# Kernel optimization log

Measured on AMD Instinct MI355X. Metric: run time of the kernel, lower is better.

The kernel has to match this reference:

```python
import jax, jax.numpy as jnp
import numpy as np

P = 32            # patch_num_row
KS = 5            # kernel_size
DIM = 1024
HEADS = 16
DIM_HEAD = 64
INNER = HEADS * DIM_HEAD
SCALE = DIM_HEAD ** -0.5


def _nearby_mask(p=P, ks=KS):
    # True = masked out (matches torch masked_fill semantics)
    pad = ks // 2
    m = np.ones((p * p, p + 2 * pad, p + 2 * pad), dtype=bool)
    for i in range(p):
        for j in range(p):
            m[i * p + j, i:i + ks, j:j + ks] = False
    m = m[:, pad:-pad, pad:-pad].reshape(p * p, p * p)
    # F.pad(mask, (1,0,1,0), value=False): unmasked first row/col (BOS token)
    m = np.pad(m, ((1, 0), (1, 0)), constant_values=False)
    return jnp.asarray(m)  # [n, n], n = p*p + 1

NB_MASK = _nearby_mask()


def setup_inputs() -> dict:
    key = jax.random.key(0)
    ks = jax.random.split(key, 8)
    b, n = 16, P * P + 1
    s = DIM ** -0.5
    return {
        "q": jax.random.normal(ks[0], (b, n, DIM), jnp.float32),
        "k": jax.random.normal(ks[1], (b, n, DIM), jnp.float32),
        "v": jax.random.normal(ks[2], (b, n, DIM), jnp.float32),
        "Wq": jax.random.normal(ks[3], (DIM, INNER), jnp.float32) * s,
        "Wk": jax.random.normal(ks[4], (DIM, INNER), jnp.float32) * s,
        "Wv": jax.random.normal(ks[5], (DIM, INNER), jnp.float32) * s,
        "Wo": jax.random.normal(ks[6], (INNER, DIM), jnp.float32) * (INNER ** -0.5),
        "bo": jnp.zeros((DIM,), jnp.float32),
    }


def reference(q, k, v, Wq, Wk, Wv, Wo, bo):
    b, n, _ = q.shape
    h, d = HEADS, DIM_HEAD
    # projections, split heads: b n (h d) -> b h n d
    qh = (q @ Wq).reshape(b, n, h, d).transpose(0, 2, 1, 3)
    kh = (k @ Wk).reshape(b, n, h, d).transpose(0, 2, 1, 3)
    vh = (v @ Wv).reshape(b, n, h, d).transpose(0, 2, 1, 3)
    dots = jnp.einsum('bhid,bhjd->bhij', qh, kh) * SCALE
    mask_value = -jnp.finfo(dots.dtype).max
    dots = jnp.where(NB_MASK[None, None], mask_value, dots)
    attn = jax.nn.softmax(dots, axis=-1)
    out = jnp.einsum('bhij,bhjd->bhid', attn, vh)
    out = out.transpose(0, 2, 1, 3).reshape(b, n, h * d)
    return out @ Wo + bo
```

## Files before the change

### kernel.cpp

```cpp
#include <hip/hip_runtime.h>

typedef unsigned short u16;
typedef unsigned int   u32;
typedef __attribute__((ext_vector_type(8))) __bf16 bf16x8;
typedef __attribute__((ext_vector_type(4))) float   f32x4;

#define MROWS 16400
#define NPADROWS 16512
#define KD 1024
#define MATEL ((size_t)NPADROWS * KD)
#define NT 16
#define BUFSZ 16384

__device__ __forceinline__ u16 f2b(float f) {
  union { float f; u32 u; } x; x.f = f;
  return (u16)((x.u + 0x7FFFu + ((x.u >> 16) & 1u)) >> 16);
}
__device__ __forceinline__ float b2f(u16 h) {
  union { u32 u; float f; } x; x.u = ((u32)h) << 16;
  return x.f;
}

__device__ __forceinline__ void gll16(const u16* g, u16* l) {
  __builtin_amdgcn_global_load_lds(
      (const __attribute__((address_space(1))) void*)g,
      (__attribute__((address_space(3))) void*)l, 16, 0, 0);
}

__global__ __launch_bounds__(256) void k_wtrans(
    const float* __restrict__ W0, const float* __restrict__ W1,
    const float* __restrict__ W2, const float* __restrict__ W3,
    u16* __restrict__ T)
{
  __shared__ float tile[32][33];
  int z = blockIdx.z;
  const float* W = (z == 0) ? W0 : (z == 1) ? W1 : (z == 2) ? W2 : W3;
  u16* Tz = T + (size_t)z * KD * KD;
  int tx = threadIdx.x, ty = threadIdx.y;
  int k0 = blockIdx.x * 32, n0 = blockIdx.y * 32;
#pragma unroll
  for (int r = ty; r < 32; r += 8)
    tile[r][tx] = W[(size_t)(k0 + r) * KD + n0 + tx];
  __syncthreads();
#pragma unroll
  for (int r = ty; r < 32; r += 8)
    Tz[(size_t)(n0 + r) * KD + k0 + tx] = f2b(tile[tx][r]);
}

__global__ __launch_bounds__(256) void k_convert(
    const float* __restrict__ q, const float* __restrict__ k,
    const float* __restrict__ v, u16* __restrict__ dst)
{
  const size_t CH_PER_MAT = MATEL / 8;
  const size_t total = 3 * CH_PER_MAT;
  for (size_t c = (size_t)blockIdx.x * 256 + threadIdx.x; c < total;
       c += (size_t)gridDim.x * 256) {
    size_t z = c / CH_PER_MAT;
    size_t r = c - z * CH_PER_MAT;
    size_t row = r >> 7;
    int col8 = (int)(r & 127) * 8;
    u16* o = dst + z * MATEL + row * KD + col8;
    if (row < MROWS) {
      const float* s = ((z == 0) ? q : (z == 1) ? k : v) + row * KD + col8;
      float4 f0 = *(const float4*)s;
      float4 f1 = *(const float4*)(s + 4);
      ushort4 o0; o0.x = f2b(f0.x); o0.y = f2b(f0.y); o0.z = f2b(f0.z); o0.w = f2b(f0.w);
      ushort4 o1; o1.x = f2b(f1.x); o1.y = f2b(f1.y); o1.z = f2b(f1.z); o1.w = f2b(f1.w);
      *(ushort4*)o = o0; *(ushort4*)(o + 4) = o1;
    } else {
      ushort4 zz; zz.x = zz.y = zz.z = zz.w = 0;
      *(ushort4*)o = zz; *(ushort4*)(o + 4) = zz;
    }
  }
}

template<bool OUT_FP32>
__global__ __launch_bounds__(256) void k_gemm(
    const u16* __restrict__ Ab, const u16* __restrict__ Bt,
    u16* __restrict__ Cb, float* __restrict__ Cf,
    const float* __restrict__ bias, int nwg)
{
  __shared__ u16 lds[2 * BUFSZ];

  int lin = blockIdx.x;
  int cpx = nwg >> 3;
  int swz = (lin & 7) * cpx + (lin >> 3);
  int bn = swz & 7;
  int rest = swz >> 3;
  int bm = rest % 129;
  int z  = rest / 129;

  int t = threadIdx.x;
  int w = t >> 6, l = t & 63;
  int lrow = l & 15, kgrp = l >> 4;
  int wm = (w >> 1) * 64, wn = (w & 1) * 64;

  int ccl = ((t & 7) ^ ((t >> 3) & 7)) * 8;
  const u16* gA[4]; const u16* gB[4];
#pragma unroll
  for (int i = 0; i < 4; ++i) {
    int prow = i * 32 + (t >> 3);
    gA[i] = Ab + (size_t)z * MATEL + (size_t)(bm * 128 + prow) * KD + ccl;
    gB[i] = Bt + (size_t)z * (1024 * 1024) + (size_t)(bn * 128 + prow) * KD + ccl;
  }

  int aoff[4], boff[4];
#pragma unroll
  for (int fm = 0; fm < 4; ++fm)
    aoff[fm] = (wm + fm * 16 + lrow) * 64 + ((kgrp ^ (l & 7)) * 8);
#pragma unroll
  for (int fn = 0; fn < 4; ++fn)
    boff[fn] = 8192 + (wn + fn * 16 + lrow) * 64 + ((kgrp ^ (l & 7)) * 8);

  f32x4 acc[4][4] = {};

#define STAGE(B) { u16* L = lds + (B) * BUFSZ;                          \
    _Pragma("unroll")                                                   \
    for (int i = 0; i < 4; ++i) { gll16(gA[i], L + i * 2048 + w * 512); gA[i] += 64; } \
    _Pragma("unroll")                                                   \
    for (int i = 0; i < 4; ++i) { gll16(gB[i], L + 8192 + i * 2048 + w * 512); gB[i] += 64; } }

  STAGE(0);
  __syncthreads();

  int buf = 0;
#pragma unroll 2
  for (int kt = 0; kt < NT; ++kt) {
    if (kt + 1 < NT) STAGE(buf ^ 1);

    const u16* Lb = lds + buf * BUFSZ;
#pragma unroll
    for (int ks = 0; ks < 2; ++ks) {
      bf16x8 af[4], bfr[4];
#pragma unroll
      for (int fm = 0; fm < 4; ++fm)
        af[fm] = *(const bf16x8*)(Lb + (aoff[fm] ^ (ks << 5)));
#pragma unroll
      for (int fn = 0; fn < 4; ++fn)
        bfr[fn] = *(const bf16x8*)(Lb + (boff[fn] ^ (ks << 5)));
#pragma unroll
      for (int fm = 0; fm < 4; ++fm)
#pragma unroll
        for (int fn = 0; fn < 4; ++fn)
          acc[fm][fn] = __builtin_amdgcn_mfma_f32_16x16x32_bf16(af[fm], bfr[fn], acc[fm][fn], 0, 0, 0);
    }

    __syncthreads();
    buf ^= 1;
  }
#undef STAGE

#pragma unroll
  for (int fm = 0; fm < 4; ++fm) {
#pragma unroll
    for (int fn = 0; fn < 4; ++fn) {
      int gcol = bn * 128 + wn + fn * 16 + lrow;
#pragma unroll
      for (int r = 0; r < 4; ++r) {
        int grow = bm * 128 + wm + fm * 16 + kgrp * 4 + r;
        if constexpr (OUT_FP32) {
          if (grow < MROWS)
            Cf[(size_t)grow * KD + gcol] = acc[fm][fn][r] + bias[gcol];
        } else {
          Cb[(size_t)z * MATEL + (size_t)grow * KD + gcol] = f2b(acc[fm][fn][r]);
        }
      }
    }
  }
}

__global__ __launch_bounds__(256) void k_attn_nb22(
    const u16* __restrict__ Qp, const u16* __restrict__ Kp,
    const u16* __restrict__ Vp, u16* __restrict__ AO)
{
  __shared__ float qrow[4][1024];
  __shared__ float dots[4][16][37];
  __shared__ float probs[4][16][37];
  __shared__ int   keys[37];
  __shared__ unsigned long long incm[4];

  int t = threadIdx.x;
  int b = blockIdx.x >> 8;
  int tile = blockIdx.x & 255;
  int pi0 = (tile >> 4) * 2, pj0 = (tile & 15) * 2;
  size_t rowbase = (size_t)b * 1025;

  int iq[4];
#pragma unroll
  for (int qi = 0; qi < 4; ++qi)
    iq[qi] = 1 + (pi0 + (qi >> 1)) * 32 + (pj0 + (qi & 1));

  {
    int qi = t >> 6, off = (t & 63) * 16;
    const u16* qp = Qp + (rowbase + iq[qi]) * 1024 + off;
    uint4 a0 = *(const uint4*)qp;
    uint4 a1 = *(const uint4*)(qp + 8);
    u32 uu[8] = {a0.x, a0.y, a0.z, a0.w, a1.x, a1.y, a1.z, a1.w};
#pragma unroll
    for (int u = 0; u < 8; ++u) {
      qrow[qi][off + u * 2]     = __uint_as_float(uu[u] << 16);
      qrow[qi][off + u * 2 + 1] = __uint_as_float(uu[u] & 0xffff0000u);
    }
  }
  if (t < 37) {
    if (t < 36) {
      int r = pi0 - 2 + t / 6, c = pj0 - 2 + t % 6;
      keys[t] = (r >= 0 && r < 32 && c >= 0 && c < 32) ? (1 + r * 32 + c) : -1;
    } else {
      keys[36] = 0;
    }
  }
  if (t < 4) {
    int di = t >> 1, dj = t & 1;
    unsigned long long m = 1ull << 36;
    for (int j = 0; j < 36; ++j) {
      int wr = j / 6, wc = j % 6;
      if (wr >= di && wr < di + 5 && wc >= dj && wc < dj + 5) m |= 1ull << j;
    }
    incm[t] = m;
  }
  __syncthreads();

  int e = t & 3;
  int hD = (t >> 2) & 15;
  float qreg[4][16];
#pragma unroll
  for (int qi = 0; qi < 4; ++qi)
#pragma unroll
    for (int u = 0; u < 16; ++u)
      qreg[qi][u] = qrow[qi][hD * 64 + e * 16 + u];

#pragma unroll
  for (int p = 0; p < 10; ++p) {
    int idx = p * 64 + (t >> 2);
    float s0 = 0.f, s1 = 0.f, s2 = 0.f, s3 = 0.f;
    int key = -1;
    if (idx < 592) {
      int j = idx >> 4;
      key = keys[j];
      if (key >= 0) {
        const u16* kp = Kp + (rowbase + key) * 1024 + hD * 64 + e * 16;
        uint4 kv0 = *(const uint4*)kp;
        uint4 kv1 = *(const uint4*)(kp + 8);
        u32 uu[8] = {kv0.x, kv0.y, kv0.z, kv0.w, kv1.x, kv1.y, kv1.z, kv1.w};
#pragma unroll
        for (int u = 0; u < 8; ++u) {
          float lo = __uint_as_float(uu[u] << 16);
          float hi = __uint_as_float(uu[u] & 0xffff0000u);
          s0 += qreg[0][u * 2] * lo + qreg[0][u * 2 + 1] * hi;
          s1 += qreg[1][u * 2] * lo + qreg[1][u * 2 + 1] * hi;
          s2 += qreg[2][u * 2] * lo + qreg[2][u * 2 + 1] * hi;
          s3 += qreg[3][u * 2] * lo + qreg[3][u * 2 + 1] * hi;
        }
      }
    }
    s0 += __shfl_xor(s0, 1); s0 += __shfl_xor(s0, 2);
    s1 += __shfl_xor(s1, 1); s1 += __shfl_xor(s1, 2);
    s2 += __shfl_xor(s2, 1); s2 += __shfl_xor(s2, 2);
    s3 += __shfl_xor(s3, 1); s3 += __shfl_xor(s3, 2);
    if (idx < 592) {
      int j = idx >> 4;
      float sv = (e == 0) ? s0 : (e == 1) ? s1 : (e == 2) ? s2 : s3;
      dots[e][hD][j] = (key >= 0) ? sv * 0.125f : -3.0e38f;
    }
  }
  __syncthreads();

  {
    int row = t >> 2;
    int qi = row >> 4, hh = row & 15;
    unsigned long long inc = incm[qi];
    float dv[10];
    float m = -3.0e38f;
#pragma unroll
    for (int s = 0; s < 10; ++s) {
      int j = e + s * 4;
      float d = -3.0e38f;
      if (j < 37) {
        d = dots[qi][hh][j];
        if (!((inc >> j) & 1)) d = -3.0e38f;
      }
      dv[s] = d;
      m = fmaxf(m, d);
    }
    m = fmaxf(m, __shfl_xor(m, 1));
    m = fmaxf(m, __shfl_xor(m, 2));
    float sum = 0.f;
    float pv[10];
#pragma unroll
    for (int s = 0; s < 10; ++s) {
      int j = e + s * 4;
      float p = (j < 37) ? __expf(dv[s] - m) : 0.f;
      pv[s] = p; sum += p;
    }
    sum += __shfl_xor(sum, 1);
    sum += __shfl_xor(sum, 2);
    float inv = 1.f / sum;
#pragma unroll
    for (int s = 0; s < 10; ++s) {
      int j = e + s * 4;
      if (j < 37) probs[qi][hh][j] = pv[s] * inv;
    }
  }
  __syncthreads();

  {
    int h = t >> 4;
    int c0 = t * 4;
    float a[4][4] = {};
    for (int j = 0; j < 37; ++j) {
      int key = keys[j];
      if (key < 0) continue;
      ushort4 vv = *(const ushort4*)(Vp + (rowbase + key) * 1024 + c0);
      float v0 = b2f(vv.x), v1 = b2f(vv.y), v2 = b2f(vv.z), v3 = b2f(vv.w);
#pragma unroll
      for (int qi = 0; qi < 4; ++qi) {
        float p = probs[qi][h][j];
        a[qi][0] += p * v0; a[qi][1] += p * v1;
        a[qi][2] += p * v2; a[qi][3] += p * v3;
      }
    }
#pragma unroll
    for (int qi = 0; qi < 4; ++qi) {
      ushort4 o;
      o.x = f2b(a[qi][0]); o.y = f2b(a[qi][1]);
      o.z = f2b(a[qi][2]); o.w = f2b(a[qi][3]);
      *(ushort4*)&AO[(rowbase + iq[qi]) * 1024 + c0] = o;
    }
  }
}

__global__ __launch_bounds__(256) void k_attn_row0(
    const u16* __restrict__ Qp, const u16* __restrict__ Kp,
    const u16* __restrict__ Vp, u16* __restrict__ AO)
{
  __shared__ float q0[64];
  __shared__ float pr[1025];
  __shared__ float red[256];
  int t = threadIdx.x;
  int b = blockIdx.x >> 4, h = blockIdx.x & 15;
  size_t rowbase = (size_t)b * 1025;

  if (t < 64) q0[t] = b2f(Qp[rowbase * 1024 + h * 64 + t]);
  __syncthreads();

  float lmax = -3.0e38f;
  for (int j = t; j < 1025; j += 256) {
    const u16* kp = Kp + (rowbase + j) * 1024 + h * 64;
    float s = 0.f;
#pragma unroll
    for (int e = 0; e < 64; e += 4) {
      ushort4 kv = *(const ushort4*)(kp + e);
      s += q0[e + 0] * b2f(kv.x) + q0[e + 1] * b2f(kv.y)
         + q0[e + 2] * b2f(kv.z) + q0[e + 3] * b2f(kv.w);
    }
    s *= 0.125f;
    pr[j] = s;
    lmax = fmaxf(lmax, s);
  }
  red[t] = lmax; __syncthreads();
  for (int s = 128; s > 0; s >>= 1) {
    if (t < s) red[t] = fmaxf(red[t], red[t + s]);
    __syncthreads();
  }
  float m = red[0]; __syncthreads();

  float lsum = 0.f;
  for (int j = t; j < 1025; j += 256) {
    float p = __expf(pr[j] - m);
    pr[j] = p; lsum += p;
  }
  red[t] = lsum; __syncthreads();
  for (int s = 128; s > 0; s >>= 1) {
    if (t < s) red[t] += red[t + s];
    __syncthreads();
  }
  float inv = 1.f / red[0]; __syncthreads();

  int d = t & 63, grp = t >> 6;
  float a = 0.f;
  for (int j = grp; j < 1025; j += 4)
    a += pr[j] * b2f(Vp[(rowbase + j) * 1024 + h * 64 + d]);
  red[t] = a; __syncthreads();
  if (t < 64) {
    float tot = (red[t] + red[t + 64]) + (red[t + 128] + red[t + 192]);
    AO[rowbase * 1024 + h * 64 + t] = f2b(tot * inv);
  }
}

extern "C" void kernel_launch(void* const* d_in, const int* in_sizes, int n_in,
                              void* d_out, int out_size, void* d_ws, size_t ws_size,
                              hipStream_t stream) {
  const float* q  = (const float*)d_in[0];
  const float* k  = (const float*)d_in[1];
  const float* v  = (const float*)d_in[2];
  const float* Wq = (const float*)d_in[3];
  const float* Wk = (const float*)d_in[4];
  const float* Wv = (const float*)d_in[5];
  const float* Wo = (const float*)d_in[6];
  const float* bo = (const float*)d_in[7];
  float* out = (float*)d_out;

  u16* wt = (u16*)d_ws;
  u16* qb = wt + (size_t)4 * 1024 * 1024;
  u16* Qp = qb + 3 * MATEL;
  u16* Kp = Qp + MATEL;
  u16* Vp = Kp + MATEL;
  u16* AO = qb;

  k_wtrans<<<dim3(32, 32, 4), dim3(32, 8), 0, stream>>>(Wq, Wk, Wv, Wo, wt);
  k_convert<<<2048, 256, 0, stream>>>(q, k, v, qb);

  k_gemm<false><<<3096, 256, 0, stream>>>(qb, wt, Qp, nullptr, nullptr, 3096);

  k_attn_nb22<<<4096, 256, 0, stream>>>(Qp, Kp, Vp, AO);
  k_attn_row0<<<256, 256, 0, stream>>>(Qp, Kp, Vp, AO);

  k_gemm<true><<<1032, 256, 0, stream>>>(AO, wt + (size_t)3 * 1024 * 1024,
                                         nullptr, out, bo, 1032);
}
```

Measured before the change: 433.2 us.

## Use 256x256 GEMM tiles with 512 threads and triple-buffered LDS pipeline

Replaces the 128x128 GEMM tile (256 threads, double buffer, K-step 64) with a 256x256 tile computed by 8 waves, K-step 32 and a three-stage LDS ring. Explicit vmcnt waits and raw barriers let two loads stay in flight, s_setprio raises MFMA priority, and an XCD-aware workgroup remap handles grid sizes not divisible by 8. The aim is more reuse of each loaded tile and better hiding of global-load latency. In exchange the block count drops to 780 and 260, which may underfill the GPU for the output projection, and register pressure rises with 32 accumulators per thread.

New measurement: 457.0 us. +5.5%, slower.

```diff
diff --git a/kernel.cpp b/kernel.cpp
--- a/kernel.cpp
+++ b/kernel.cpp
@@ -9,8 +9,6 @@
 #define NPADROWS 16512
 #define KD 1024
 #define MATEL ((size_t)NPADROWS * KD)
-#define NT 16
-#define BUFSZ 16384
 
 __device__ __forceinline__ u16 f2b(float f) {
   union { float f; u32 u; } x; x.f = f;
@@ -75,94 +73,115 @@
 }
 
 template<bool OUT_FP32>
-__global__ __launch_bounds__(256) void k_gemm(
+__global__ __launch_bounds__(512, 1) void k_gemm(
     const u16* __restrict__ Ab, const u16* __restrict__ Bt,
     u16* __restrict__ Cb, float* __restrict__ Cf,
     const float* __restrict__ bias, int nwg)
 {
-  __shared__ u16 lds[2 * BUFSZ];
+  __shared__ u16 lds[3 * 16384];
 
   int lin = blockIdx.x;
-  int cpx = nwg >> 3;
-  int swz = (lin & 7) * cpx + (lin >> 3);
-  int bn = swz & 7;
-  int rest = swz >> 3;
-  int bm = rest % 129;
-  int z  = rest / 129;
+  int qq = nwg >> 3, r8 = nwg & 7;
+  int xcd = lin & 7, pos = lin >> 3;
+  int wg = (xcd < r8 ? xcd * (qq + 1) : r8 * (qq + 1) + (xcd - r8) * qq) + pos;
+  int bn = wg & 3;
+  int rest = wg >> 2;
+  int bm = rest % 65;
+  int z  = rest / 65;
 
   int t = threadIdx.x;
   int w = t >> 6, l = t & 63;
   int lrow = l & 15, kgrp = l >> 4;
-  int wm = (w >> 1) * 64, wn = (w & 1) * 64;
-
-  int ccl = ((t & 7) ^ ((t >> 3) & 7)) * 8;
-  const u16* gA[4]; const u16* gB[4];
-#pragma unroll
-  for (int i = 0; i < 4; ++i) {
-    int prow = i * 32 + (t >> 3);
-    gA[i] = Ab + (size_t)z * MATEL + (size_t)(bm * 128 + prow) * KD + ccl;
-    gB[i] = Bt + (size_t)z * (1024 * 1024) + (size_t)(bn * 128 + prow) * KD + ccl;
-  }
-
-  int aoff[4], boff[4];
-#pragma unroll
-  for (int fm = 0; fm < 4; ++fm)
-    aoff[fm] = (wm + fm * 16 + lrow) * 64 + ((kgrp ^ (l & 7)) * 8);
-#pragma unroll
-  for (int fn = 0; fn < 4; ++fn)
-    boff[fn] = 8192 + (wn + fn * 16 + lrow) * 64 + ((kgrp ^ (l & 7)) * 8);
-
-  f32x4 acc[4][4] = {};
-
-#define STAGE(B) { u16* L = lds + (B) * BUFSZ;                          \
+  int wrow = w >> 2, wcol = w & 3;
+
+  int ccl = ((t & 3) ^ ((t >> 2) & 3)) * 8;
+  int pr = t >> 2;
+  int ar0 = bm * 256 + pr;        if (ar0 > NPADROWS - 1) ar0 = NPADROWS - 1;
+  int ar1 = bm * 256 + 128 + pr;  if (ar1 > NPADROWS - 1) ar1 = NPADROWS - 1;
+  const u16* gA0 = Ab + (size_t)z * MATEL + (size_t)ar0 * KD + ccl;
+  const u16* gA1 = Ab + (size_t)z * MATEL + (size_t)ar1 * KD + ccl;
+  const u16* gB0 = Bt + (size_t)z * (1024 * 1024) + (size_t)(bn * 256 + pr) * KD + ccl;
+  const u16* gB1 = gB0 + (size_t)128 * KD;
+
+  int xk = (kgrp ^ (lrow & 3)) * 8;
+  int abase = (wrow * 128 + lrow) * 32 + xk;
+  int bbase = 8192 + (wcol * 64 + lrow) * 32 + xk;
+
+  f32x4 acc[8][4] = {};
+
+#define STAGE(B) { u16* L = lds + (B) * 16384;                          \
+    gll16(gA0, L + w * 512);          gll16(gA1, L + 4096 + w * 512);   \
+    gll16(gB0, L + 8192 + w * 512);   gll16(gB1, L + 12288 + w * 512);  \
+    gA0 += 32; gA1 += 32; gB0 += 32; gB1 += 32; }
+
+#define WAITV4 do { __builtin_amdgcn_sched_barrier(0);                  \
+    asm volatile("s_waitcnt vmcnt(4)" ::: "memory");                    \
+    __builtin_amdgcn_sched_barrier(0); } while (0)
+#define WAITV0 do { __builtin_amdgcn_sched_barrier(0);                  \
+    asm volatile("s_waitcnt vmcnt(0)" ::: "memory");                    \
+    __builtin_amdgcn_sched_barrier(0); } while (0)
+#define BAR do { __builtin_amdgcn_s_barrier();                          \
+    __builtin_amdgcn_sched_barrier(0); } while (0)
+
+#define TILE_BODY(CUR) {                                                \
+    const u16* Lb = lds + (CUR) * 16384;                                \
+    bf16x8 bfr[4];                                                      \
     _Pragma("unroll")                                                   \
-    for (int i = 0; i < 4; ++i) { gll16(gA[i], L + i * 2048 + w * 512); gA[i] += 64; } \
+    for (int fn = 0; fn < 4; ++fn) bfr[fn] = *(const bf16x8*)(Lb + bbase + fn * 512); \
     _Pragma("unroll")                                                   \
-    for (int i = 0; i < 4; ++i) { gll16(gB[i], L + 8192 + i * 2048 + w * 512); gB[i] += 64; } }
-
-  STAGE(0);
-  __syncthreads();
-
-  int buf = 0;
-#pragma unroll 2
-  for (int kt = 0; kt < NT; ++kt) {
-    if (kt + 1 < NT) STAGE(buf ^ 1);
-
-    const u16* Lb = lds + buf * BUFSZ;
-#pragma unroll
-    for (int ks = 0; ks < 2; ++ks) {
-      bf16x8 af[4], bfr[4];
-#pragma unroll
-      for (int fm = 0; fm < 4; ++fm)
-        af[fm] = *(const bf16x8*)(Lb + (aoff[fm] ^ (ks << 5)));
-#pragma unroll
-      for (int fn = 0; fn < 4; ++fn)
-        bfr[fn] = *(const bf16x8*)(Lb + (boff[fn] ^ (ks << 5)));
-#pragma unroll
-      for (int fm = 0; fm < 4; ++fm)
-#pragma unroll
-        for (int fn = 0; fn < 4; ++fn)
-          acc[fm][fn] = __builtin_amdgcn_mfma_f32_16x16x32_bf16(af[fm], bfr[fn], acc[fm][fn], 0, 0, 0);
-    }
-
-    __syncthreads();
-    buf ^= 1;
+    for (int fh = 0; fh < 2; ++fh) {                                    \
+      bf16x8 af[4];                                                     \
+      _Pragma("unroll")                                                 \
+      for (int fq = 0; fq < 4; ++fq)                                    \
+        af[fq] = *(const bf16x8*)(Lb + abase + (fh * 4 + fq) * 512);    \
+      __builtin_amdgcn_s_setprio(1);                                    \
+      _Pragma("unroll")                                                 \
+      for (int fq = 0; fq < 4; ++fq)                                    \
+        _Pragma("unroll")                                               \
+        for (int fn = 0; fn < 4; ++fn)                                  \
+          acc[fh * 4 + fq][fn] = __builtin_amdgcn_mfma_f32_16x16x32_bf16( \
+              af[fq], bfr[fn], acc[fh * 4 + fq][fn], 0, 0, 0);          \
+      __builtin_amdgcn_s_setprio(0);                                    \
+    } }
+
+  STAGE(0); STAGE(1);
+  WAITV4;
+  BAR;
+
+  int cur = 0;
+  for (int kt = 0; kt < 32; ++kt) {
+    if (kt + 2 < 32) {
+      int pre = cur + 2; if (pre >= 3) pre -= 3;
+      STAGE(pre);
+    }
+    TILE_BODY(cur);
+    if (kt + 1 < 32) {
+      if (kt + 2 < 32) { WAITV4; }
+      else            { WAITV0; }
+      BAR;
+    }
+    cur += 1; if (cur == 3) cur = 0;
   }
 #undef STAGE
-
-#pragma unroll
-  for (int fm = 0; fm < 4; ++fm) {
+#undef TILE_BODY
+#undef WAITV4
+#undef WAITV0
+#undef BAR
+
+#pragma unroll
+  for (int fm = 0; fm < 8; ++fm) {
 #pragma unroll
     for (int fn = 0; fn < 4; ++fn) {
-      int gcol = bn * 128 + wn + fn * 16 + lrow;
+      int gcol = bn * 256 + wcol * 64 + fn * 16 + lrow;
 #pragma unroll
       for (int r = 0; r < 4; ++r) {
-        int grow = bm * 128 + wm + fm * 16 + kgrp * 4 + r;
+        int grow = bm * 256 + wrow * 128 + fm * 16 + kgrp * 4 + r;
         if constexpr (OUT_FP32) {
           if (grow < MROWS)
             Cf[(size_t)grow * KD + gcol] = acc[fm][fn][r] + bias[gcol];
         } else {
-          Cb[(size_t)z * MATEL + (size_t)grow * KD + gcol] = f2b(acc[fm][fn][r]);
+          if (grow < NPADROWS)
+            Cb[(size_t)z * MATEL + (size_t)grow * KD + gcol] = f2b(acc[fm][fn][r]);
         }
       }
     }
@@ -411,11 +430,11 @@
   k_wtrans<<<dim3(32, 32, 4), dim3(32, 8), 0, stream>>>(Wq, Wk, Wv, Wo, wt);
   k_convert<<<2048, 256, 0, stream>>>(q, k, v, qb);
 
-  k_gemm<false><<<3096, 256, 0, stream>>>(qb, wt, Qp, nullptr, nullptr, 3096);
+  k_gemm<false><<<780, 512, 0, stream>>>(qb, wt, Qp, nullptr, nullptr, 780);
 
   k_attn_nb22<<<4096, 256, 0, stream>>>(Qp, Kp, Vp, AO);
   k_attn_row0<<<256, 256, 0, stream>>>(Qp, Kp, Vp, AO);
 
-  k_gemm<true><<<1032, 256, 0, stream>>>(AO, wt + (size_t)3 * 1024 * 1024,
-                                         nullptr, out, bo, 1032);
-}
+  k_gemm<true><<<260, 512, 0, stream>>>(AO, wt + (size_t)3 * 1024 * 1024,
+                                        nullptr, out, bo, 260);
+}
```

## Fuse fp32-to-bf16 input conversion into QKV GEMM and merge attention kernels

Applied to the files above, without the earlier changes.

Removes the separate conversion pass over q/k/v. The QKV GEMM now loads fp32 activations straight into LDS via global_load_lds and converts them to bf16 while building MFMA fragments. This avoids writing and re-reading a bf16 copy of the inputs, but it doubles the A-tile bytes moved per K step and adds conversion ALU work inside the GEMM loop, with a smaller K tile (32). The two attention kernels are also merged into one launch that branches on block index, saving a launch and letting the BOS-row blocks overlap with the neighbourhood blocks.

Result: slower. 446.8 us (+3.1%).

```diff
diff --git a/kernel.cpp b/kernel.cpp
--- a/kernel.cpp
+++ b/kernel.cpp
@@ -9,8 +9,6 @@
 #define NPADROWS 16512
 #define KD 1024
 #define MATEL ((size_t)NPADROWS * KD)
-#define NT 16
-#define BUFSZ 16384
 
 __device__ __forceinline__ u16 f2b(float f) {
   union { float f; u32 u; } x; x.f = f;
@@ -21,7 +19,7 @@
   return x.f;
 }
 
-__device__ __forceinline__ void gll16(const u16* g, u16* l) {
+__device__ __forceinline__ void gll16(const void* g, u16* l) {
   __builtin_amdgcn_global_load_lds(
       (const __attribute__((address_space(1))) void*)g,
       (__attribute__((address_space(3))) void*)l, 16, 0, 0);
@@ -47,40 +45,12 @@
     Tz[(size_t)(n0 + r) * KD + k0 + tx] = f2b(tile[tx][r]);
 }
 
-__global__ __launch_bounds__(256) void k_convert(
-    const float* __restrict__ q, const float* __restrict__ k,
-    const float* __restrict__ v, u16* __restrict__ dst)
+__global__ __launch_bounds__(256) void k_gemm_qkv(
+    const float* __restrict__ Aq, const float* __restrict__ Ak,
+    const float* __restrict__ Av, const u16* __restrict__ Bt,
+    u16* __restrict__ Cb, int nwg)
 {
-  const size_t CH_PER_MAT = MATEL / 8;
-  const size_t total = 3 * CH_PER_MAT;
-  for (size_t c = (size_t)blockIdx.x * 256 + threadIdx.x; c < total;
-       c += (size_t)gridDim.x * 256) {
-    size_t z = c / CH_PER_MAT;
-    size_t r = c - z * CH_PER_MAT;
-    size_t row = r >> 7;
-    int col8 = (int)(r & 127) * 8;
-    u16* o = dst + z * MATEL + row * KD + col8;
-    if (row < MROWS) {
-      const float* s = ((z == 0) ? q : (z == 1) ? k : v) + row * KD + col8;
-      float4 f0 = *(const float4*)s;
-      float4 f1 = *(const float4*)(s + 4);
-      ushort4 o0; o0.x = f2b(f0.x); o0.y = f2b(f0.y); o0.z = f2b(f0.z); o0.w = f2b(f0.w);
-      ushort4 o1; o1.x = f2b(f1.x); o1.y = f2b(f1.y); o1.z = f2b(f1.z); o1.w = f2b(f1.w);
-      *(ushort4*)o = o0; *(ushort4*)(o + 4) = o1;
-    } else {
-      ushort4 zz; zz.x = zz.y = zz.z = zz.w = 0;
-      *(ushort4*)o = zz; *(ushort4*)(o + 4) = zz;
-    }
-  }
-}
-
-template<bool OUT_FP32>
-__global__ __launch_bounds__(256) void k_gemm(
-    const u16* __restrict__ Ab, const u16* __restrict__ Bt,
-    u16* __restrict__ Cb, float* __restrict__ Cf,
-    const float* __restrict__ bias, int nwg)
-{
-  __shared__ u16 lds[2 * BUFSZ];
+  __shared__ u16 lds[2 * 12288];
 
   int lin = blockIdx.x;
   int cpx = nwg >> 3;
@@ -89,12 +59,109 @@
   int rest = swz >> 3;
   int bm = rest % 129;
   int z  = rest / 129;
+  const float* Af = (z == 0) ? Aq : (z == 1) ? Ak : Av;
 
   int t = threadIdx.x;
   int w = t >> 6, l = t & 63;
   int lrow = l & 15, kgrp = l >> 4;
   int wm = (w >> 1) * 64, wn = (w & 1) * 64;
 
+  int acol = ((t & 7) ^ ((t >> 3) & 7)) * 4;
+  const float* gA[4];
+#pragma unroll
+  for (int i = 0; i < 4; ++i) {
+    int row = bm * 128 + i * 32 + (t >> 3);
+    if (row > MROWS - 1) row = MROWS - 1;
+    gA[i] = Af + (size_t)row * KD + acol;
+  }
+  int srow = w * 16 + (l >> 2);
+  int scolB = ((l & 3) ^ ((l >> 2) & 3)) * 8;
+  const u16* gB  = Bt + (size_t)z * (1024 * 1024) + (size_t)(bn * 128 + srow) * KD + scolB;
+  const u16* gB2 = gB + (size_t)64 * KD;
+  int dB0 = 8192 + w * 512;
+  int dB1 = 8192 + 2048 + w * 512;
+
+  f32x4 acc[4][4] = {};
+
+#define STAGEQ(B) { u16* L = lds + (B) * 12288;                         \
+    _Pragma("unroll")                                                   \
+    for (int i = 0; i < 4; ++i) { gll16(gA[i], L + i * 2048 + w * 512); gA[i] += 32; } \
+    gll16(gB, L + dB0); gll16(gB2, L + dB1); gB += 32; gB2 += 32; }
+
+  STAGEQ(0);
+  __syncthreads();
+
+  int buf = 0;
+#pragma unroll 2
+  for (int kt = 0; kt < 32; ++kt) {
+    if (kt + 1 < 32) STAGEQ(buf ^ 1);
+
+    const u16* Lb = lds + buf * 12288;
+    const float* LA = (const float*)Lb;
+    bf16x8 af[4], bfr[4];
+    int x7 = lrow & 7;
+#pragma unroll
+    for (int fm = 0; fm < 4; ++fm) {
+      int rb = (wm + fm * 16 + lrow) * 32;
+      f32x4 lo = *(const f32x4*)(LA + rb + (((2 * kgrp)     ^ x7) * 4));
+      f32x4 hi = *(const f32x4*)(LA + rb + (((2 * kgrp + 1) ^ x7) * 4));
+      bf16x8 v;
+      v[0] = (__bf16)lo[0]; v[1] = (__bf16)lo[1];
+      v[2] = (__bf16)lo[2]; v[3] = (__bf16)lo[3];
+      v[4] = (__bf16)hi[0]; v[5] = (__bf16)hi[1];
+      v[6] = (__bf16)hi[2]; v[7] = (__bf16)hi[3];
+      af[fm] = v;
+    }
+#pragma unroll
+    for (int fn = 0; fn < 4; ++fn)
+      bfr[fn] = *(const bf16x8*)(Lb + 8192 + (wn + fn * 16 + lrow) * 32
+                                 + ((kgrp ^ (lrow & 3)) * 8));
+#pragma unroll
+    for (int fm = 0; fm < 4; ++fm)
+#pragma unroll
+      for (int fn = 0; fn < 4; ++fn)
+        acc[fm][fn] = __builtin_amdgcn_mfma_f32_16x16x32_bf16(af[fm], bfr[fn], acc[fm][fn], 0, 0, 0);
+
+    __syncthreads();
+    buf ^= 1;
+  }
+#undef STAGEQ
+
+#pragma unroll
+  for (int fm = 0; fm < 4; ++fm) {
+#pragma unroll
+    for (int fn = 0; fn < 4; ++fn) {
+      int gcol = bn * 128 + wn + fn * 16 + lrow;
+#pragma unroll
+      for (int r = 0; r < 4; ++r) {
+        int grow = bm * 128 + wm + fm * 16 + kgrp * 4 + r;
+        Cb[(size_t)z * MATEL + (size_t)grow * KD + gcol] = f2b(acc[fm][fn][r]);
+      }
+    }
+  }
+}
+
+template<bool OUT_FP32>
+__global__ __launch_bounds__(256) void k_gemm(
+    const u16* __restrict__ Ab, const u16* __restrict__ Bt,
+    u16* __restrict__ Cb, float* __restrict__ Cf,
+    const float* __restrict__ bias, int nwg)
+{
+  __shared__ u16 lds[2 * 16384];
+
+  int lin = blockIdx.x;
+  int cpx = nwg >> 3;
+  int swz = (lin & 7) * cpx + (lin >> 3);
+  int bn = swz & 7;
+  int rest = swz >> 3;
+  int bm = rest % 129;
+  int z  = rest / 129;
+
+  int t = threadIdx.x;
+  int w = t >> 6, l = t & 63;
+  int lrow = l & 15, kgrp = l >> 4;
+  int wm = (w >> 1) * 64, wn = (w & 1) * 64;
+
   int ccl = ((t & 7) ^ ((t >> 3) & 7)) * 8;
   const u16* gA[4]; const u16* gB[4];
 #pragma unroll
@@ -114,7 +181,7 @@
 
   f32x4 acc[4][4] = {};
 
-#define STAGE(B) { u16* L = lds + (B) * BUFSZ;                          \
+#define STAGE(B) { u16* L = lds + (B) * 16384;                          \
     _Pragma("unroll")                                                   \
     for (int i = 0; i < 4; ++i) { gll16(gA[i], L + i * 2048 + w * 512); gA[i] += 64; } \
     _Pragma("unroll")                                                   \
@@ -125,10 +192,10 @@
 
   int buf = 0;
 #pragma unroll 2
-  for (int kt = 0; kt < NT; ++kt) {
-    if (kt + 1 < NT) STAGE(buf ^ 1);
-
-    const u16* Lb = lds + buf * BUFSZ;
+  for (int kt = 0; kt < 16; ++kt) {
+    if (kt + 1 < 16) STAGE(buf ^ 1);
+
+    const u16* Lb = lds + buf * 16384;
 #pragma unroll
     for (int ks = 0; ks < 2; ++ks) {
       bf16x8 af[4], bfr[4];
@@ -169,222 +236,220 @@
   }
 }
 
-__global__ __launch_bounds__(256) void k_attn_nb22(
+__global__ __launch_bounds__(256) void k_attn(
     const u16* __restrict__ Qp, const u16* __restrict__ Kp,
     const u16* __restrict__ Vp, u16* __restrict__ AO)
 {
-  __shared__ float qrow[4][1024];
-  __shared__ float dots[4][16][37];
-  __shared__ float probs[4][16][37];
-  __shared__ int   keys[37];
-  __shared__ unsigned long long incm[4];
-
   int t = threadIdx.x;
-  int b = blockIdx.x >> 8;
-  int tile = blockIdx.x & 255;
-  int pi0 = (tile >> 4) * 2, pj0 = (tile & 15) * 2;
-  size_t rowbase = (size_t)b * 1025;
-
-  int iq[4];
-#pragma unroll
-  for (int qi = 0; qi < 4; ++qi)
-    iq[qi] = 1 + (pi0 + (qi >> 1)) * 32 + (pj0 + (qi & 1));
-
-  {
-    int qi = t >> 6, off = (t & 63) * 16;
-    const u16* qp = Qp + (rowbase + iq[qi]) * 1024 + off;
-    uint4 a0 = *(const uint4*)qp;
-    uint4 a1 = *(const uint4*)(qp + 8);
-    u32 uu[8] = {a0.x, a0.y, a0.z, a0.w, a1.x, a1.y, a1.z, a1.w};
-#pragma unroll
-    for (int u = 0; u < 8; ++u) {
-      qrow[qi][off + u * 2]     = __uint_as_float(uu[u] << 16);
-      qrow[qi][off + u * 2 + 1] = __uint_as_float(uu[u] & 0xffff0000u);
-    }
-  }
-  if (t < 37) {
-    if (t < 36) {
-      int r = pi0 - 2 + t / 6, c = pj0 - 2 + t % 6;
-      keys[t] = (r >= 0 && r < 32 && c >= 0 && c < 32) ? (1 + r * 32 + c) : -1;
-    } else {
-      keys[36] = 0;
-    }
-  }
-  if (t < 4) {
-    int di = t >> 1, dj = t & 1;
-    unsigned long long m = 1ull << 36;
-    for (int j = 0; j < 36; ++j) {
-      int wr = j / 6, wc = j % 6;
-      if (wr >= di && wr < di + 5 && wc >= dj && wc < dj + 5) m |= 1ull << j;
-    }
-    incm[t] = m;
-  }
-  __syncthreads();
-
-  int e = t & 3;
-  int hD = (t >> 2) & 15;
-  float qreg[4][16];
-#pragma unroll
-  for (int qi = 0; qi < 4; ++qi)
-#pragma unroll
-    for (int u = 0; u < 16; ++u)
-      qreg[qi][u] = qrow[qi][hD * 64 + e * 16 + u];
-
-#pragma unroll
-  for (int p = 0; p < 10; ++p) {
-    int idx = p * 64 + (t >> 2);
-    float s0 = 0.f, s1 = 0.f, s2 = 0.f, s3 = 0.f;
-    int key = -1;
-    if (idx < 592) {
-      int j = idx >> 4;
-      key = keys[j];
-      if (key >= 0) {
-        const u16* kp = Kp + (rowbase + key) * 1024 + hD * 64 + e * 16;
-        uint4 kv0 = *(const uint4*)kp;
-        uint4 kv1 = *(const uint4*)(kp + 8);
-        u32 uu[8] = {kv0.x, kv0.y, kv0.z, kv0.w, kv1.x, kv1.y, kv1.z, kv1.w};
-#pragma unroll
-        for (int u = 0; u < 8; ++u) {
-          float lo = __uint_as_float(uu[u] << 16);
-          float hi = __uint_as_float(uu[u] & 0xffff0000u);
-          s0 += qreg[0][u * 2] * lo + qreg[0][u * 2 + 1] * hi;
-          s1 += qreg[1][u * 2] * lo + qreg[1][u * 2 + 1] * hi;
-          s2 += qreg[2][u * 2] * lo + qreg[2][u * 2 + 1] * hi;
-          s3 += qreg[3][u * 2] * lo + qreg[3][u * 2 + 1] * hi;
+
+  if (blockIdx.x < 4096) {
+    __shared__ float qrow[4][1024];
+    __shared__ float dots[4][16][37];
+    __shared__ float probs[4][16][37];
+    __shared__ int   keys[37];
+    __shared__ unsigned long long incm[4];
+
+    int b = blockIdx.x >> 8;
+    int tile = blockIdx.x & 255;
+    int pi0 = (tile >> 4) * 2, pj0 = (tile & 15) * 2;
+    size_t rowbase = (size_t)b * 1025;
+
+    int iq[4];
+#pragma unroll
+    for (int qi = 0; qi < 4; ++qi)
+      iq[qi] = 1 + (pi0 + (qi >> 1)) * 32 + (pj0 + (qi & 1));
+
+    {
+      int qi = t >> 6, off = (t & 63) * 16;
+      const u16* qp = Qp + (rowbase + iq[qi]) * 1024 + off;
+      uint4 a0 = *(const uint4*)qp;
+      uint4 a1 = *(const uint4*)(qp + 8);
+      u32 uu[8] = {a0.x, a0.y, a0.z, a0.w, a1.x, a1.y, a1.z, a1.w};
+#pragma unroll
+      for (int u = 0; u < 8; ++u) {
+        qrow[qi][off + u * 2]     = __uint_as_float(uu[u] << 16);
+        qrow[qi][off + u * 2 + 1] = __uint_as_float(uu[u] & 0xffff0000u);
+      }
+    }
+    if (t < 37) {
+      if (t < 36) {
+        int r = pi0 - 2 + t / 6, c = pj0 - 2 + t % 6;
+        keys[t] = (r >= 0 && r < 32 && c >= 0 && c < 32) ? (1 + r * 32 + c) : -1;
+      } else {
+        keys[36] = 0;
+      }
+    }
+    if (t < 4) {
+      int di = t >> 1, dj = t & 1;
+      unsigned long long m = 1ull << 36;
+      for (int j = 0; j < 36; ++j) {
+        int wr = j / 6, wc = j % 6;
+        if (wr >= di && wr < di + 5 && wc >= dj && wc < dj + 5) m |= 1ull << j;
+      }
+      incm[t] = m;
+    }
+    __syncthreads();
+
+    int e = t & 3;
+    int hD = (t >> 2) & 15;
+    float qreg[4][16];
+#pragma unroll
+    for (int qi = 0; qi < 4; ++qi)
+#pragma unroll
+      for (int u = 0; u < 16; ++u)
+        qreg[qi][u] = qrow[qi][hD * 64 + e * 16 + u];
+
+#pragma unroll
+    for (int p = 0; p < 10; ++p) {
+      int idx = p * 64 + (t >> 2);
+      float s0 = 0.f, s1 = 0.f, s2 = 0.f, s3 = 0.f;
+      int key = -1;
+      if (idx < 592) {
+        int j = idx >> 4;
+        key = keys[j];
+        if (key >= 0) {
+          const u16* kp = Kp + (rowbase + key) * 1024 + hD * 64 + e * 16;
+          uint4 kv0 = *(const uint4*)kp;
+          uint4 kv1 = *(const uint4*)(kp + 8);
+          u32 uu[8] = {kv0.x, kv0.y, kv0.z, kv0.w, kv1.x, kv1.y, kv1.z, kv1.w};
+#pragma unroll
+          for (int u = 0; u < 8; ++u) {
+            float lo = __uint_as_float(uu[u] << 16);
+            float hi = __uint_as_float(uu[u] & 0xffff0000u);
+            s0 += qreg[0][u * 2] * lo + qreg[0][u * 2 + 1] * hi;
+            s1 += qreg[1][u * 2] * lo + qreg[1][u * 2 + 1] * hi;
+            s2 += qreg[2][u * 2] * lo + qreg[2][u * 2 + 1] * hi;
+            s3 += qreg[3][u * 2] * lo + qreg[3][u * 2 + 1] * hi;
+          }
         }
       }
-    }
-    s0 += __shfl_xor(s0, 1); s0 += __shfl_xor(s0, 2);
-    s1 += __shfl_xor(s1, 1); s1 += __shfl_xor(s1, 2);
-    s2 += __shfl_xor(s2, 1); s2 += __shfl_xor(s2, 2);
-    s3 += __shfl_xor(s3, 1); s3 += __shfl_xor(s3, 2);
-    if (idx < 592) {
-      int j = idx >> 4;
-      float sv = (e == 0) ? s0 : (e == 1) ? s1 : (e == 2) ? s2 : s3;
-      dots[e][hD][j] = (key >= 0) ? sv * 0.125f : -3.0e38f;
-    }
-  }
-  __syncthreads();
-
-  {
-    int row = t >> 2;
-    int qi = row >> 4, hh = row & 15;
-    unsigned long long inc = incm[qi];
-    float dv[10];
-    float m = -3.0e38f;
-#pragma unroll
-    for (int s = 0; s < 10; ++s) {
-      int j = e + s * 4;
-      float d = -3.0e38f;
-      if (j < 37) {
-        d = dots[qi][hh][j];
-        if (!((inc >> j) & 1)) d = -3.0e38f;
-      }
-      dv[s] = d;
-      m = fmaxf(m, d);
-    }
-    m = fmaxf(m, __shfl_xor(m, 1));
-    m = fmaxf(m, __shfl_xor(m, 2));
-    float sum = 0.f;
-    float pv[10];
-#pragma unroll
-    for (int s = 0; s < 10; ++s) {
-      int j = e + s * 4;
-      float p = (j < 37) ? __expf(dv[s] - m) : 0.f;
-      pv[s] = p; sum += p;
-    }
-    sum += __shfl_xor(sum, 1);
-    sum += __shfl_xor(sum, 2);
-    float inv = 1.f / sum;
-#pragma unroll
-    for (int s = 0; s < 10; ++s) {
-      int j = e + s * 4;
-      if (j < 37) probs[qi][hh][j] = pv[s] * inv;
-    }
-  }
-  __syncthreads();
-
-  {
-    int h = t >> 4;
-    int c0 = t * 4;
-    float a[4][4] = {};
-    for (int j = 0; j < 37; ++j) {
-      int key = keys[j];
-      if (key < 0) continue;
-      ushort4 vv = *(const ushort4*)(Vp + (rowbase + key) * 1024 + c0);
-      float v0 = b2f(vv.x), v1 = b2f(vv.y), v2 = b2f(vv.z), v3 = b2f(vv.w);
+      s0 += __shfl_xor(s0, 1); s0 += __shfl_xor(s0, 2);
+      s1 += __shfl_xor(s1, 1); s1 += __shfl_xor(s1, 2);
+      s2 += __shfl_xor(s2, 1); s2 += __shfl_xor(s2, 2);
+      s3 += __shfl_xor(s3, 1); s3 += __shfl_xor(s3, 2);
+      if (idx < 592) {
+        int j = idx >> 4;
+        float sv = (e == 0) ? s0 : (e == 1) ? s1 : (e == 2) ? s2 : s3;
+        dots[e][hD][j] = (key >= 0) ? sv * 0.125f : -3.0e38f;
+      }
+    }
+    __syncthreads();
+
+    {
+      int row = t >> 2;
+      int qi = row >> 4, hh = row & 15;
+      unsigned long long inc = incm[qi];
+      float dv[10];
+      float m = -3.0e38f;
+#pragma unroll
+      for (int s = 0; s < 10; ++s) {
+        int j = e + s * 4;
+        float d = -3.0e38f;
+        if (j < 37) {
+          d = dots[qi][hh][j];
+          if (!((inc >> j) & 1)) d = -3.0e38f;
+        }
+        dv[s] = d;
+        m = fmaxf(m, d);
+      }
+      m = fmaxf(m, __shfl_xor(m, 1));
+      m = fmaxf(m, __shfl_xor(m, 2));
+      float sum = 0.f;
+      float pv[10];
+#pragma unroll
+      for (int s = 0; s < 10; ++s) {
+        int j = e + s * 4;
+        float p = (j < 37) ? __expf(dv[s] - m) : 0.f;
+        pv[s] = p; sum += p;
+      }
+      sum += __shfl_xor(sum, 1);
+      sum += __shfl_xor(sum, 2);
+      float inv = 1.f / sum;
+#pragma unroll
+      for (int s = 0; s < 10; ++s) {
+        int j = e + s * 4;
+        if (j < 37) probs[qi][hh][j] = pv[s] * inv;
+      }
+    }
+    __syncthreads();
+
+    {
+      int h = t >> 4;
+      int c0 = t * 4;
+      float a[4][4] = {};
+      for (int j = 0; j < 37; ++j) {
+        int key = keys[j];
+        if (key < 0) continue;
+        ushort4 vv = *(const ushort4*)(Vp + (rowbase + key) * 1024 + c0);
+        float v0 = b2f(vv.x), v1 = b2f(vv.y), v2 = b2f(vv.z), v3 = b2f(vv.w);
+#pragma unroll
+        for (int qi = 0; qi < 4; ++qi) {
+          float p = probs[qi][h][j];
+          a[qi][0] += p * v0; a[qi][1] += p * v1;
+          a[qi][2] += p * v2; a[qi][3] += p * v3;
+        }
+      }
 #pragma unroll
       for (int qi = 0; qi < 4; ++qi) {
-        float p = probs[qi][h][j];
-        a[qi][0] += p * v0; a[qi][1] += p * v1;
-        a[qi][2] += p * v2; a[qi][3] += p * v3;
-      }
-    }
-#pragma unroll
-    for (int qi = 0; qi < 4; ++qi) {
-      ushort4 o;
-      o.x = f2b(a[qi][0]); o.y = f2b(a[qi][1]);
-      o.z = f2b(a[qi][2]); o.w = f2b(a[qi][3]);
-      *(ushort4*)&AO[(rowbase + iq[qi]) * 1024 + c0] = o;
-    }
-  }
-}
-
-__global__ __launch_bounds__(256) void k_attn_row0(
-    const u16* __restrict__ Qp, const u16* __restrict__ Kp,
-    const u16* __restrict__ Vp, u16* __restrict__ AO)
-{
-  __shared__ float q0[64];
-  __shared__ float pr[1025];
-  __shared__ float red[256];
-  int t = threadIdx.x;
-  int b = blockIdx.x >> 4, h = blockIdx.x & 15;
-  size_t rowbase = (size_t)b * 1025;
-
-  if (t < 64) q0[t] = b2f(Qp[rowbase * 1024 + h * 64 + t]);
-  __syncthreads();
-
-  float lmax = -3.0e38f;
-  for (int j = t; j < 1025; j += 256) {
-    const u16* kp = Kp + (rowbase + j) * 1024 + h * 64;
-    float s = 0.f;
-#pragma unroll
-    for (int e = 0; e < 64; e += 4) {
-      ushort4 kv = *(const ushort4*)(kp + e);
-      s += q0[e + 0] * b2f(kv.x) + q0[e + 1] * b2f(kv.y)
-         + q0[e + 2] * b2f(kv.z) + q0[e + 3] * b2f(kv.w);
-    }
-    s *= 0.125f;
-    pr[j] = s;
-    lmax = fmaxf(lmax, s);
-  }
-  red[t] = lmax; __syncthreads();
-  for (int s = 128; s > 0; s >>= 1) {
-    if (t < s) red[t] = fmaxf(red[t], red[t + s]);
-    __syncthreads();
-  }
-  float m = red[0]; __syncthreads();
-
-  float lsum = 0.f;
-  for (int j = t; j < 1025; j += 256) {
-    float p = __expf(pr[j] - m);
-    pr[j] = p; lsum += p;
-  }
-  red[t] = lsum; __syncthreads();
-  for (int s = 128; s > 0; s >>= 1) {
-    if (t < s) red[t] += red[t + s];
-    __syncthreads();
-  }
-  float inv = 1.f / red[0]; __syncthreads();
-
-  int d = t & 63, grp = t >> 6;
-  float a = 0.f;
-  for (int j = grp; j < 1025; j += 4)
-    a += pr[j] * b2f(Vp[(rowbase + j) * 1024 + h * 64 + d]);
-  red[t] = a; __syncthreads();
-  if (t < 64) {
-    float tot = (red[t] + red[t + 64]) + (red[t + 128] + red[t + 192]);
-    AO[rowbase * 1024 + h * 64 + t] = f2b(tot * inv);
+        ushort4 o;
+        o.x = f2b(a[qi][0]); o.y = f2b(a[qi][1]);
+        o.z = f2b(a[qi][2]); o.w = f2b(a[qi][3]);
+        *(ushort4*)&AO[(rowbase + iq[qi]) * 1024 + c0] = o;
+      }
+    }
+  } else {
+    __shared__ float q0[64];
+    __shared__ float pr[1025];
+    __shared__ float red[256];
+    int bid = blockIdx.x - 4096;
+    int b = bid >> 4, h = bid & 15;
+    size_t rowbase = (size_t)b * 1025;
+
+    if (t < 64) q0[t] = b2f(Qp[rowbase * 1024 + h * 64 + t]);
+    __syncthreads();
+
+    float lmax = -3.0e38f;
+    for (int j = t; j < 1025; j += 256) {
+      const u16* kp = Kp + (rowbase + j) * 1024 + h * 64;
+      float s = 0.f;
+#pragma unroll
+      for (int e = 0; e < 64; e += 4) {
+        ushort4 kv = *(const ushort4*)(kp + e);
+        s += q0[e + 0] * b2f(kv.x) + q0[e + 1] * b2f(kv.y)
+           + q0[e + 2] * b2f(kv.z) + q0[e + 3] * b2f(kv.w);
+      }
+      s *= 0.125f;
+      pr[j] = s;
+      lmax = fmaxf(lmax, s);
+    }
+    red[t] = lmax; __syncthreads();
+    for (int s = 128; s > 0; s >>= 1) {
+      if (t < s) red[t] = fmaxf(red[t], red[t + s]);
+      __syncthreads();
+    }
+    float m = red[0]; __syncthreads();
+
+    float lsum = 0.f;
+    for (int j = t; j < 1025; j += 256) {
+      float p = __expf(pr[j] - m);
+      pr[j] = p; lsum += p;
+    }
+    red[t] = lsum; __syncthreads();
+    for (int s = 128; s > 0; s >>= 1) {
+      if (t < s) red[t] += red[t + s];
+      __syncthreads();
+    }
+    float inv = 1.f / red[0]; __syncthreads();
+
+    int d = t & 63, grp = t >> 6;
+    float a = 0.f;
+    for (int j = grp; j < 1025; j += 4)
+      a += pr[j] * b2f(Vp[(rowbase + j) * 1024 + h * 64 + d]);
+    red[t] = a; __syncthreads();
+    if (t < 64) {
+      float tot = (red[t] + red[t + 64]) + (red[t + 128] + red[t + 192]);
+      AO[rowbase * 1024 + h * 64 + t] = f2b(tot * inv);
+    }
   }
 }
 
@@ -402,19 +467,16 @@
   float* out = (float*)d_out;
 
   u16* wt = (u16*)d_ws;
-  u16* qb = wt + (size_t)4 * 1024 * 1024;
-  u16* Qp = qb + 3 * MATEL;
+  u16* AO = wt + (size_t)4 * 1024 * 1024;
+  u16* Qp = AO + MATEL;
   u16* Kp = Qp + MATEL;
   u16* Vp = Kp + MATEL;
-  u16* AO = qb;
 
   k_wtrans<<<dim3(32, 32, 4), dim3(32, 8), 0, stream>>>(Wq, Wk, Wv, Wo, wt);
-  k_convert<<<2048, 256, 0, stream>>>(q, k, v, qb);
-
-  k_gemm<false><<<3096, 256, 0, stream>>>(qb, wt, Qp, nullptr, nullptr, 3096);
-
-  k_attn_nb22<<<4096, 256, 0, stream>>>(Qp, Kp, Vp, AO);
-  k_attn_row0<<<256, 256, 0, stream>>>(Qp, Kp, Vp, AO);
+
+  k_gemm_qkv<<<3096, 256, 0, stream>>>(q, k, v, wt, Qp, 3096);
+
+  k_attn<<<4352, 256, 0, stream>>>(Qp, Kp, Vp, AO);
 
   k_gemm<true><<<1032, 256, 0, stream>>>(AO, wt + (size_t)3 * 1024 * 1024,
                                          nullptr, out, bo, 1032);
```
